# Optimization experiments

Measured on AMD Instinct MI355X. Metric: run time of the kernel, lower is better.

## Reference

```python
import jax, jax.numpy as jnp
import numpy as np

H = 1024     # hidden_size
NH = 16      # num heads
HD = H // NH # head_dim = 64
I = 4096     # intermediate_size
EPS = 1e-6


def rmsnorm(x, w, eps=EPS):
    var = jnp.mean(jnp.square(x), axis=-1, keepdims=True)
    return x * jax.lax.rsqrt(var + eps) * w


def attention(x, ctx, wq, wk, wv, wo):
    # x: [B,S,H], ctx: [B,Skv,H]; weights stored [in,out]
    B, S, _ = x.shape
    Skv = ctx.shape[1]
    q = (x @ wq).reshape(B, S, NH, HD)
    k = (ctx @ wk).reshape(B, Skv, NH, HD)
    v = (ctx @ wv).reshape(B, Skv, NH, HD)
    scores = jnp.einsum('bqhd,bkhd->bhqk', q, k) * (HD ** -0.5)
    attn = jax.nn.softmax(scores.astype(jnp.float32), axis=-1).astype(q.dtype)
    out = jnp.einsum('bhqk,bkhd->bqhd', attn, v).reshape(B, S, NH * HD)
    return out @ wo


def mlp(x, wg, wu, wd):
    return (jax.nn.silu(x @ wg) * (x @ wu)) @ wd


def setup_inputs() -> dict:
    key = jax.random.key(0)
    ks = jax.random.split(key, 16)
    p = lambda k, shape: (jax.random.normal(k, shape, jnp.float32) * 0.02)
    return {
        'hidden_states': jax.random.normal(ks[0], (1, 2048, H), jnp.float32),
        'context': jax.random.normal(ks[1], (1, 2048, H), jnp.float32),
        'sa_norm_w': jnp.ones((H,), jnp.float32),
        'sa_wq': p(ks[2], (H, NH * HD)),
        'sa_wk': p(ks[3], (H, NH * HD)),
        'sa_wv': p(ks[4], (H, NH * HD)),
        'sa_wo': p(ks[5], (NH * HD, H)),
        'ca_norm_w': jnp.ones((H,), jnp.float32),
        'ca_wq': p(ks[6], (H, NH * HD)),
        'ca_wk': p(ks[7], (H, NH * HD)),
        'ca_wv': p(ks[8], (H, NH * HD)),
        'ca_wo': p(ks[9], (NH * HD, H)),
        'mlp_norm_w': jnp.ones((H,), jnp.float32),
        'w_gate': p(ks[10], (H, I)),
        'w_up': p(ks[11], (H, I)),
        'w_down': p(ks[12], (I, H)),
    }


def reference(hidden_states, context, sa_norm_w, sa_wq, sa_wk, sa_wv, sa_wo,
              ca_norm_w, ca_wq, ca_wk, ca_wv, ca_wo,
              mlp_norm_w, w_gate, w_up, w_down):
    # self-attention block
    residual = hidden_states
    h = rmsnorm(hidden_states, sa_norm_w)
    h = residual + attention(h, h, sa_wq, sa_wk, sa_wv, sa_wo)
    # cross-attention block
    residual = h
    hn = rmsnorm(h, ca_norm_w)
    h = residual + attention(hn, context, ca_wq, ca_wk, ca_wv, ca_wo)
    # MLP block
    residual = h
    hn = rmsnorm(h, mlp_norm_w)
    h = residual + mlp(hn, w_gate, w_up, w_down)
    return h
```

## Files before the change

### kernel.cpp

```cpp
#include <hip/hip_runtime.h>

#define H 1024
#define S 2048
#define NH 16
#define HD 64
#define ISZ 4096

typedef __attribute__((ext_vector_type(8))) short s8v;
typedef __attribute__((ext_vector_type(4))) short s4v;
typedef __attribute__((ext_vector_type(4))) float f4v;

__device__ __forceinline__ short f2bf(float f) {
    unsigned u = __builtin_bit_cast(unsigned, f);
    unsigned r = (u + 0x7FFFu + ((u >> 16) & 1u)) >> 16;
    return (short)r;
}
__device__ __forceinline__ float bf2f(short s) {
    unsigned u = ((unsigned)(unsigned short)s) << 16;
    return __builtin_bit_cast(float, u);
}

__device__ __forceinline__ void gload_lds16(const short* g, short* l) {
    __builtin_amdgcn_global_load_lds(
        (const __attribute__((address_space(1))) void*)g,
        (__attribute__((address_space(3))) void*)l, 16, 0, 0);
}

struct PreArgs {
    const void* hid; const void* ctx;
    const void* sanw; const void* canw; const void* mlpnw;
    const void* w[11];
    short* hidc; short* ctxc; short* xn;
    short* canw_o; short* mlpnw_o;
    short* wT[11];
    int* flag_out;
};

__device__ __forceinline__ void tr_tile(const void* src, short* dst, int K, int N,
                                        int k0, int n0, int rmul, int roff,
                                        int isbf, float* tile ) {
    int t = threadIdx.x;
    int c = t & 31, r0 = t >> 5;
    if (isbf) {
        const short* s = (const short*)src;
#pragma unroll
        for (int i = 0; i < 4; i++)
            tile[(r0 + i * 8) * 33 + c] = bf2f(s[(k0 + r0 + i * 8) * N + n0 + c]);
    } else {
        const float* s = (const float*)src;
#pragma unroll
        for (int i = 0; i < 4; i++)
            tile[(r0 + i * 8) * 33 + c] = s[(k0 + r0 + i * 8) * N + n0 + c];
    }
    __syncthreads();
#pragma unroll
    for (int i = 0; i < 4; i++)
        dst[((n0 + r0 + i * 8) * rmul + roff) * K + k0 + c] = f2bf(tile[c * 33 + r0 + i * 8]);
}

__global__ __launch_bounds__(256) void preamble_kernel(PreArgs pa) {
    __shared__ float tile[32 * 33];
    __shared__ float red[4];
    int b = blockIdx.x;
    int t = threadIdx.x;
    int isbf = (((const unsigned*)pa.sanw)[0] == 0x3F803F80u);
    if (blockIdx.x == 0 && t == 0) pa.flag_out[0] = isbf;

    if (b < 2048) {
        int row = b;
        float xf[4];
        if (isbf) {
            s4v xv = *(const s4v*)((const short*)pa.hid + row * H + t * 4);
#pragma unroll
            for (int j = 0; j < 4; j++) xf[j] = bf2f(xv[j]);
        } else {
            const float* s = (const float*)pa.hid + row * H + t * 4;
#pragma unroll
            for (int j = 0; j < 4; j++) xf[j] = s[j];
        }
        float ss = 0.f;
        s4v cv;
#pragma unroll
        for (int j = 0; j < 4; j++) { cv[j] = f2bf(xf[j]); xf[j] = bf2f(cv[j]); ss += xf[j] * xf[j]; }
        *(s4v*)(pa.hidc + row * H + t * 4) = cv;
        int lane = t & 63, wid = t >> 6;
#pragma unroll
        for (int off = 32; off >= 1; off >>= 1) ss += __shfl_xor(ss, off);
        if (lane == 0) red[wid] = ss;
        __syncthreads();
        float tot = red[0] + red[1] + red[2] + red[3];
        float scale = rsqrtf(tot * (1.f / (float)H) + 1e-6f);
        float wv[4];
        if (isbf) {
            s4v wq = *(const s4v*)((const short*)pa.sanw + t * 4);
#pragma unroll
            for (int j = 0; j < 4; j++) wv[j] = bf2f(wq[j]);
        } else {
            const float* s = (const float*)pa.sanw + t * 4;
#pragma unroll
            for (int j = 0; j < 4; j++) wv[j] = s[j];
        }
        s4v ov;
#pragma unroll
        for (int j = 0; j < 4; j++) ov[j] = f2bf(xf[j] * scale * wv[j]);
        *(s4v*)(pa.xn + row * H + t * 4) = ov;
        return;
    }
    b -= 2048;
    if (b < 1024) {
        int i8 = b * 2048 + t * 8;
        if (isbf) {
            *(s8v*)(pa.ctxc + i8) = *(const s8v*)((const short*)pa.ctx + i8);
        } else {
            const float* s = (const float*)pa.ctx;
            s8v o;
#pragma unroll
            for (int j = 0; j < 8; j++) o[j] = f2bf(s[i8 + j]);
            *(s8v*)(pa.ctxc + i8) = o;
        }
        return;
    }
    b -= 1024;
    if (b < 2) {
        const void* src = (b == 0) ? pa.canw : pa.mlpnw;
        short* dst = (b == 0) ? pa.canw_o : pa.mlpnw_o;
        if (isbf) { if (t * 4 < H) *(s4v*)(dst + t * 4) = *(const s4v*)((const short*)src + t * 4); }
        else {
            const float* s = (const float*)src;
            s4v o;
#pragma unroll
            for (int j = 0; j < 4; j++) o[j] = f2bf(s[t * 4 + j]);
            *(s4v*)(dst + t * 4) = o;
        }
        return;
    }
    b -= 2;
    if (b < 8 * 1024) {
        int w = b >> 10, tl = b & 1023;
        tr_tile(pa.w[w], pa.wT[w], H, H, (tl & 31) * 32, (tl >> 5) * 32, 1, 0, isbf, tile);
        return;
    }
    b -= 8 * 1024;
    if (b < 2 * 4096) {
        int w = 8 + (b >> 12), tl = b & 4095;
        tr_tile(pa.w[w], pa.wT[8], H, ISZ, (tl & 31) * 32, (tl >> 5) * 32, 2, w - 8, isbf, tile);
        return;
    }
    b -= 2 * 4096;
    {
        tr_tile(pa.w[10], pa.wT[10], ISZ, H, (b & 127) * 32, (b >> 7) * 32, 1, 0, isbf, tile);
    }
}

__global__ __launch_bounds__(256) void rmsnorm_kernel(const short* __restrict__ x,
                                                      const short* __restrict__ w,
                                                      short* __restrict__ out) {
    int row = blockIdx.x;
    int t = threadIdx.x;
    int lane = t & 63, wid = t >> 6;
    const short* xr = x + row * H;

    s4v xv = *(const s4v*)(xr + t * 4);
    float xf[4];
    float ss = 0.f;
#pragma unroll
    for (int j = 0; j < 4; j++) { xf[j] = bf2f(xv[j]); ss += xf[j] * xf[j]; }
#pragma unroll
    for (int off = 32; off >= 1; off >>= 1) ss += __shfl_xor(ss, off);

    __shared__ float red[4];
    if (lane == 0) red[wid] = ss;
    __syncthreads();
    float tot = red[0] + red[1] + red[2] + red[3];
    float scale = rsqrtf(tot * (1.f / (float)H) + 1e-6f);

    s4v wv = *(const s4v*)(w + t * 4);
    s4v ov;
#pragma unroll
    for (int j = 0; j < 4; j++) ov[j] = f2bf(xf[j] * scale * bf2f(wv[j]));
    *(s4v*)(out + row * H + t * 4) = ov;
}

template <int BM_, int BN_>
__global__ __launch_bounds__(256, 2) void gemm_bt_kernel(
    const short* __restrict__ A0, const short* __restrict__ A1, int split, int lda,
    const short* __restrict__ Bt,
    void* __restrict__ C, int ldc, int K,
    const short* __restrict__ res,
    const int* __restrict__ dtype_flag,
    short* __restrict__ vtbuf, int vcol0,
    short* __restrict__ silu_out) {

    constexpr int MC = BM_ / 32;
    constexpr int NC = BN_ / 32;

    const short* A = (blockIdx.y < split) ? A0 : A1;
    int m0 = blockIdx.x * BM_;
    int n0 = blockIdx.y * BN_;

    __shared__ short As[2 * BM_ * 32];
    __shared__ short Bs[2 * BN_ * 32];

    int t = threadIdx.x;
    int lane = t & 63, wid = t >> 6;
    int quad = lane >> 4, l15 = lane & 15;
    int wr = wid >> 1, wc = wid & 1;

    f4v acc[MC][NC] = {};

    int ld4 = lane >> 2, lc8 = (lane & 3) * 8;

    for (int k0 = 0; k0 < K; k0 += 64) {
#pragma unroll
        for (int h = 0; h < 2; h++) {
#pragma unroll
            for (int i = 0; i < BM_ / 64; i++)
                gload_lds16(A + (m0 + wid * (BM_ / 4) + i * 16 + ld4) * lda + k0 + h * 32 + lc8,
                            As + h * BM_ * 32 + (wid * (BM_ / 4) + i * 16) * 32);
#pragma unroll
            for (int i = 0; i < BN_ / 64; i++)
                gload_lds16(Bt + (n0 + wid * (BN_ / 4) + i * 16 + ld4) * K + k0 + h * 32 + lc8,
                            Bs + h * BN_ * 32 + (wid * (BN_ / 4) + i * 16) * 32);
        }
        __syncthreads();

#pragma unroll
        for (int h = 0; h < 2; h++) {
            s8v af[MC], bfv[NC];
#pragma unroll
            for (int mc = 0; mc < MC; mc++)
                af[mc] = *(const s8v*)(As + h * BM_ * 32 + (wr * (BM_ / 2) + mc * 16 + l15) * 32 + quad * 8);
#pragma unroll
            for (int nc = 0; nc < NC; nc++)
                bfv[nc] = *(const s8v*)(Bs + h * BN_ * 32 + (wc * (BN_ / 2) + nc * 16 + l15) * 32 + quad * 8);

#pragma unroll
            for (int mc = 0; mc < MC; mc++)
#pragma unroll
                for (int nc = 0; nc < NC; nc++)
                    acc[mc][nc] = __builtin_amdgcn_mfma_f32_16x16x32_bf16(af[mc], bfv[nc], acc[mc][nc], 0, 0, 0);
        }
        __syncthreads();
    }

    if (silu_out) {
#pragma unroll
        for (int mc = 0; mc < MC; mc++) {
#pragma unroll
            for (int nc = 0; nc < NC; nc++) {
                int row = m0 + wr * (BM_ / 2) + mc * 16 + quad * 4;
                int col = n0 + wc * (BN_ / 2) + nc * 16 + l15;
#pragma unroll
                for (int r = 0; r < 4; r++) {
                    float v = acc[mc][nc][r];
                    float other = __shfl_xor(v, 1);
                    if ((l15 & 1) == 0) {
                        float sig = 1.f / (1.f + __expf(-v));
                        silu_out[(row + r) * ISZ + (col >> 1)] = f2bf(v * sig * other);
                    }
                }
            }
        }
        return;
    }

    int out_fp32 = (dtype_flag != nullptr) && (dtype_flag[0] == 0);

#pragma unroll
    for (int mc = 0; mc < MC; mc++) {
#pragma unroll
        for (int nc = 0; nc < NC; nc++) {
            int row = m0 + wr * (BM_ / 2) + mc * 16 + quad * 4;
            int col = n0 + wc * (BN_ / 2) + nc * 16 + l15;
#pragma unroll
            for (int r = 0; r < 4; r++) {
                float vf = acc[mc][nc][r];
                if (res) vf += bf2f(res[(row + r) * ldc + col]);
                if (vtbuf && col >= vcol0)
                    vtbuf[(col - vcol0) * S + row + r] = f2bf(vf);
                else if (out_fp32)
                    ((float*)C)[(row + r) * ldc + col] = vf;
                else
                    ((short*)C)[(row + r) * ldc + col] = f2bf(vf);
            }
        }
    }
}

__global__ __launch_bounds__(256) void flash_attn_kernel(const short* __restrict__ q,
                                                         const short* __restrict__ k,
                                                         const short* __restrict__ vt,
                                                         int rs,
                                                         short* __restrict__ o) {
    int h = blockIdx.y;
    int q0 = blockIdx.x * 64;
    int t = threadIdx.x;
    int lane = t & 63, wid = t >> 6;
    int quad = lane >> 4, l15 = lane & 15;

    __shared__ short K2[2 * 128 * 32];
    __shared__ short V2[4 * 64 * 32];
    __shared__ short Pw[4][2048];

    int ld4 = lane >> 2, lc8 = (lane & 3) * 8;

    s8v bq[2];
    int qrow = q0 + wid * 16 + l15;
#pragma unroll
    for (int c = 0; c < 2; c++) {
        s8v raw = *(const s8v*)(q + qrow * rs + h * HD + c * 32 + quad * 8);
#pragma unroll
        for (int j = 0; j < 8; j++) bq[c][j] = f2bf(0.125f * bf2f(raw[j]));
    }

    f4v o_acc[4] = {};
    float m_s = -INFINITY, l_s = 0.f;

    for (int kv0 = 0; kv0 < S; kv0 += 128) {
#pragma unroll
        for (int dc = 0; dc < 2; dc++)
#pragma unroll
            for (int i = 0; i < 2; i++)
                gload_lds16(k + (kv0 + wid * 32 + i * 16 + ld4) * rs + h * HD + dc * 32 + lc8,
                            K2 + dc * 4096 + (wid * 32 + i * 16) * 32);
#pragma unroll
        for (int kc2 = 0; kc2 < 4; kc2++)
            gload_lds16(vt + (h * HD + wid * 16 + ld4) * S + kv0 + kc2 * 32 + lc8,
                        V2 + kc2 * 2048 + (wid * 16) * 32);
        __syncthreads();

        f4v st[8];
#pragma unroll
        for (int kc = 0; kc < 8; kc++) {
            f4v a_ = (f4v){0.f, 0.f, 0.f, 0.f};
#pragma unroll
            for (int dc = 0; dc < 2; dc++) {
                s8v kf = *(const s8v*)(K2 + dc * 4096 + (kc * 16 + l15) * 32 + quad * 8);
                a_ = __builtin_amdgcn_mfma_f32_16x16x32_bf16(kf, bq[dc], a_, 0, 0, 0);
            }
            st[kc] = a_;
        }

        float mloc = -INFINITY;
#pragma unroll
        for (int kc = 0; kc < 8; kc++)
#pragma unroll
            for (int r = 0; r < 4; r++) mloc = fmaxf(mloc, st[kc][r]);
        mloc = fmaxf(mloc, __shfl_xor(mloc, 16));
        mloc = fmaxf(mloc, __shfl_xor(mloc, 32));
        float m_new = fmaxf(m_s, mloc);
        float alpha = __expf(m_s - m_new);
        float lloc = 0.f;
#pragma unroll
        for (int kc = 0; kc < 8; kc++)
#pragma unroll
            for (int r = 0; r < 4; r++) {
                float p = __expf(st[kc][r] - m_new);
                st[kc][r] = p;
                lloc += p;
            }
        lloc += __shfl_xor(lloc, 16);
        lloc += __shfl_xor(lloc, 32);
        l_s = l_s * alpha + lloc;
        m_s = m_new;
#pragma unroll
        for (int nd = 0; nd < 4; nd++)
#pragma unroll
            for (int r = 0; r < 4; r++) o_acc[nd][r] *= alpha;

#pragma unroll
        for (int kc = 0; kc < 8; kc++)
#pragma unroll
            for (int r = 0; r < 4; r++)
                Pw[wid][(kc >> 1) * 512 + l15 * 32 + (kc & 1) * 16 + quad * 4 + r] = f2bf(st[kc][r]);

#pragma unroll
        for (int nd = 0; nd < 4; nd++) {
#pragma unroll
            for (int kc2 = 0; kc2 < 4; kc2++) {
                s8v vf = *(const s8v*)(V2 + kc2 * 2048 + (nd * 16 + l15) * 32 + quad * 8);
                s8v pf = *(const s8v*)(Pw[wid] + kc2 * 512 + l15 * 32 + quad * 8);
                o_acc[nd] = __builtin_amdgcn_mfma_f32_16x16x32_bf16(vf, pf, o_acc[nd], 0, 0, 0);
            }
        }
        __syncthreads();
    }

    float inv = 1.f / l_s;
#pragma unroll
    for (int nd = 0; nd < 4; nd++)
#pragma unroll
        for (int r = 0; r < 4; r++)
            Pw[wid][l15 * 64 + nd * 16 + quad * 4 + r] = f2bf(o_acc[nd][r] * inv);

    int qr = lane >> 2, dc2 = (lane & 3) * 16;
    s8v x0 = *(const s8v*)(Pw[wid] + qr * 64 + dc2);
    s8v x1 = *(const s8v*)(Pw[wid] + qr * 64 + dc2 + 8);
    short* dst = o + (q0 + wid * 16 + qr) * H + h * HD + dc2;
    *(s8v*)(dst) = x0;
    *(s8v*)(dst + 8) = x1;
}

extern "C" void kernel_launch(void* const* d_in, const int* in_sizes, int n_in,
                              void* d_out, int out_size, void* d_ws, size_t ws_size,
                              hipStream_t stream) {
    const int SH = S * H;
    const int WH = H * H;
    const int WI = H * ISZ;

    int* flag = (int*)d_ws;
    short* base = (short*)d_ws + 16;

    short* hidc   = base;
    short* ctxc   = hidc + SH;
    short* sanw   = ctxc + SH;
    short* canw   = sanw + H;
    short* mlpnw  = canw + H;
    short* saqkvT = mlpnw + H;
    short* sawoT  = saqkvT + 3 * WH;
    short* caqkvT = sawoT + WH;
    short* cawoT  = caqkvT + 3 * WH;
    short* wguT   = cawoT + WH;
    short* wdT    = wguT + 2 * WI;
    short* xn     = wdT + WI;
    short* qkv    = xn + SH;
    short* ao     = qkv + 3 * SH;
    short* h1     = ao + SH;
    short* gu     = qkv;
    short* h2     = qkv + 8 * SH;
    short* vt     = h2 + SH;

    dim3 blk(256);

    PreArgs pa;
    pa.hid = d_in[0]; pa.ctx = d_in[1];
    pa.sanw = d_in[2]; pa.canw = d_in[7]; pa.mlpnw = d_in[12];
    const void* wsrc[11] = {d_in[3], d_in[4], d_in[5], d_in[6],
                            d_in[8], d_in[9], d_in[10], d_in[11],
                            d_in[13], d_in[14], d_in[15]};
    short* wdst[11] = {saqkvT, saqkvT + WH, saqkvT + 2 * WH, sawoT,
                       caqkvT, caqkvT + WH, caqkvT + 2 * WH, cawoT,
                       wguT, wguT , wdT};
    for (int i = 0; i < 11; i++) { pa.w[i] = wsrc[i]; pa.wT[i] = wdst[i]; }
    pa.hidc = hidc; pa.ctxc = ctxc; pa.xn = xn;
    pa.canw_o = canw; pa.mlpnw_o = mlpnw;
    pa.flag_out = flag;
    const int pre_blocks = 2048 + 1024 + 2 + 8 * 1024 + 2 * 4096 + 4096;
    preamble_kernel<<<pre_blocks, blk, 0, stream>>>(pa);

    gemm_bt_kernel<64, 128><<<dim3(S / 64, 3 * H / 128), blk, 0, stream>>>(
        xn, xn, 24, H, saqkvT, qkv, 3 * H, H, nullptr, nullptr, vt, 2 * H, nullptr);
    flash_attn_kernel<<<dim3(S / 64, NH), blk, 0, stream>>>(qkv, qkv + H, vt, 3 * H, ao);
    gemm_bt_kernel<64, 64><<<dim3(S / 64, H / 64), blk, 0, stream>>>(
        ao, ao, 16, H, sawoT, h1, H, H, hidc, nullptr, nullptr, 0, nullptr);

    rmsnorm_kernel<<<S, blk, 0, stream>>>(h1, canw, xn);
    gemm_bt_kernel<64, 128><<<dim3(S / 64, 3 * H / 128), blk, 0, stream>>>(
        xn, ctxc, 8, H, caqkvT, qkv, 3 * H, H, nullptr, nullptr, vt, 2 * H, nullptr);
    flash_attn_kernel<<<dim3(S / 64, NH), blk, 0, stream>>>(qkv, qkv + H, vt, 3 * H, ao);
    gemm_bt_kernel<64, 64><<<dim3(S / 64, H / 64), blk, 0, stream>>>(
        ao, ao, 16, H, cawoT, h2, H, H, h1, nullptr, nullptr, 0, nullptr);

    rmsnorm_kernel<<<S, blk, 0, stream>>>(h2, mlpnw, xn);
    gemm_bt_kernel<128, 128><<<dim3(S / 128, 2 * ISZ / 128), blk, 0, stream>>>(
        xn, xn, 64, H, wguT, nullptr, 2 * ISZ, H, nullptr, nullptr, nullptr, 0, gu);
    gemm_bt_kernel<64, 64><<<dim3(S / 64, H / 64), blk, 0, stream>>>(
        gu, gu, 16, ISZ, wdT, d_out, H, ISZ, h2, flag, nullptr, 0, nullptr);
}
```

Before: 499.3 us.

## Double-buffer GEMM LDS tiles, use 8-wave blocks and larger tiles

Rewrites the GEMM kernel to use 512-thread blocks with a 2x4 wave layout and a double-buffered LDS ping-pong. The next K-tile is loaded while the current one is computed, so there is one barrier per iteration instead of two. Tile sizes grow at every call site (128x128 for QKV, 64x128 for the out/down projections, 256x256 for gate/up). The goal is to hide global-load latency and raise data reuse per block. The cost is more LDS and register pressure per block: 256x256 needs 128 KB of LDS plus 32 accumulator tiles per wave, which may cut occupancy or exceed the LDS limit. The larger tiles also give fewer blocks for the small GEMMs.

```diff
diff --git a/kernel.cpp b/kernel.cpp
--- a/kernel.cpp
+++ b/kernel.cpp
@@ -182,7 +182,7 @@
 }
 
 template <int BM_, int BN_>
-__global__ __launch_bounds__(256, 2) void gemm_bt_kernel(
+__global__ __launch_bounds__(512, 2) void gemm_bt_kernel(
     const short* __restrict__ A0, const short* __restrict__ A1, int split, int lda,
     const short* __restrict__ Bt,
     void* __restrict__ C, int ldc, int K,
@@ -192,56 +192,73 @@
     short* __restrict__ silu_out) {
 
     constexpr int MC = BM_ / 32;
-    constexpr int NC = BN_ / 32;
+    constexpr int NC = BN_ / 64;
+    constexpr int U  = (BM_ + BN_) / 8;
+    constexpr int PT = U / 8;
+    constexpr int BUF = (BM_ + BN_) * 64;
+
+    __shared__ short lds[2 * BUF];
 
     const short* A = (blockIdx.y < split) ? A0 : A1;
     int m0 = blockIdx.x * BM_;
     int n0 = blockIdx.y * BN_;
 
-    __shared__ short As[2 * BM_ * 32];
-    __shared__ short Bs[2 * BN_ * 32];
-
     int t = threadIdx.x;
     int lane = t & 63, wid = t >> 6;
     int quad = lane >> 4, l15 = lane & 15;
-    int wr = wid >> 1, wc = wid & 1;
+    int wr = wid >> 2, wc = wid & 3;
+    int ld4 = lane >> 2, lc8 = (lane & 3) * 8;
 
     f4v acc[MC][NC] = {};
 
-    int ld4 = lane >> 2, lc8 = (lane & 3) * 8;
-
-    for (int k0 = 0; k0 < K; k0 += 64) {
-#pragma unroll
-        for (int h = 0; h < 2; h++) {
-#pragma unroll
-            for (int i = 0; i < BM_ / 64; i++)
-                gload_lds16(A + (m0 + wid * (BM_ / 4) + i * 16 + ld4) * lda + k0 + h * 32 + lc8,
-                            As + h * BM_ * 32 + (wid * (BM_ / 4) + i * 16) * 32);
-#pragma unroll
-            for (int i = 0; i < BN_ / 64; i++)
-                gload_lds16(Bt + (n0 + wid * (BN_ / 4) + i * 16 + ld4) * K + k0 + h * 32 + lc8,
-                            Bs + h * BN_ * 32 + (wid * (BN_ / 4) + i * 16) * 32);
-        }
+    auto stage = [&](short* buf, int k0) {
+#pragma unroll
+        for (int s = 0; s < PT; ++s) {
+            int u = wid * PT + s;
+            if (u < BM_ / 8) {
+                int h = u / (BM_ / 16), r16 = u % (BM_ / 16);
+                gload_lds16(A + (m0 + r16 * 16 + ld4) * lda + k0 + h * 32 + lc8,
+                            buf + h * (BM_ * 32) + r16 * 512);
+            } else {
+                int ub = u - BM_ / 8;
+                int h = ub / (BN_ / 16), r16 = ub % (BN_ / 16);
+                gload_lds16(Bt + (n0 + r16 * 16 + ld4) * K + k0 + h * 32 + lc8,
+                            buf + BM_ * 64 + h * (BN_ * 32) + r16 * 512);
+            }
+        }
+    };
+
+    auto compute = [&](const short* buf) {
+#pragma unroll
+        for (int kh = 0; kh < 2; ++kh) {
+            s8v af[MC], bfv[NC];
+#pragma unroll
+            for (int mc = 0; mc < MC; ++mc)
+                af[mc] = *(const s8v*)(buf + kh * (BM_ * 32) +
+                                       (wr * (BM_ / 2) + mc * 16 + l15) * 32 + quad * 8);
+#pragma unroll
+            for (int nc = 0; nc < NC; ++nc)
+                bfv[nc] = *(const s8v*)(buf + BM_ * 64 + kh * (BN_ * 32) +
+                                        (wc * (BN_ / 4) + nc * 16 + l15) * 32 + quad * 8);
+#pragma unroll
+            for (int mc = 0; mc < MC; ++mc)
+#pragma unroll
+                for (int nc = 0; nc < NC; ++nc)
+                    acc[mc][nc] = __builtin_amdgcn_mfma_f32_16x16x32_bf16(af[mc], bfv[nc], acc[mc][nc], 0, 0, 0);
+        }
+    };
+
+    const int KT = K / 64;
+    stage(lds, 0);
+    __syncthreads();
+    int cur = 0;
+    for (int kt = 0; kt < KT - 1; ++kt) {
+        stage(lds + (cur ^ 1) * BUF, (kt + 1) * 64);
+        compute(lds + cur * BUF);
         __syncthreads();
-
-#pragma unroll
-        for (int h = 0; h < 2; h++) {
-            s8v af[MC], bfv[NC];
-#pragma unroll
-            for (int mc = 0; mc < MC; mc++)
-                af[mc] = *(const s8v*)(As + h * BM_ * 32 + (wr * (BM_ / 2) + mc * 16 + l15) * 32 + quad * 8);
-#pragma unroll
-            for (int nc = 0; nc < NC; nc++)
-                bfv[nc] = *(const s8v*)(Bs + h * BN_ * 32 + (wc * (BN_ / 2) + nc * 16 + l15) * 32 + quad * 8);
-
-#pragma unroll
-            for (int mc = 0; mc < MC; mc++)
-#pragma unroll
-                for (int nc = 0; nc < NC; nc++)
-                    acc[mc][nc] = __builtin_amdgcn_mfma_f32_16x16x32_bf16(af[mc], bfv[nc], acc[mc][nc], 0, 0, 0);
-        }
-        __syncthreads();
-    }
+        cur ^= 1;
+    }
+    compute(lds + cur * BUF);
 
     if (silu_out) {
 #pragma unroll
@@ -249,7 +266,7 @@
 #pragma unroll
             for (int nc = 0; nc < NC; nc++) {
                 int row = m0 + wr * (BM_ / 2) + mc * 16 + quad * 4;
-                int col = n0 + wc * (BN_ / 2) + nc * 16 + l15;
+                int col = n0 + wc * (BN_ / 4) + nc * 16 + l15;
 #pragma unroll
                 for (int r = 0; r < 4; r++) {
                     float v = acc[mc][nc][r];
@@ -271,7 +288,7 @@
 #pragma unroll
         for (int nc = 0; nc < NC; nc++) {
             int row = m0 + wr * (BM_ / 2) + mc * 16 + quad * 4;
-            int col = n0 + wc * (BN_ / 2) + nc * 16 + l15;
+            int col = n0 + wc * (BN_ / 4) + nc * 16 + l15;
 #pragma unroll
             for (int r = 0; r < 4; r++) {
                 float vf = acc[mc][nc][r];
@@ -431,6 +448,7 @@
     short* vt     = h2 + SH;
 
     dim3 blk(256);
+    dim3 blk2(512);
 
     PreArgs pa;
     pa.hid = d_in[0]; pa.ctx = d_in[1];
@@ -448,22 +466,22 @@
     const int pre_blocks = 2048 + 1024 + 2 + 8 * 1024 + 2 * 4096 + 4096;
     preamble_kernel<<<pre_blocks, blk, 0, stream>>>(pa);
 
-    gemm_bt_kernel<64, 128><<<dim3(S / 64, 3 * H / 128), blk, 0, stream>>>(
+    gemm_bt_kernel<128, 128><<<dim3(S / 128, 3 * H / 128), blk2, 0, stream>>>(
         xn, xn, 24, H, saqkvT, qkv, 3 * H, H, nullptr, nullptr, vt, 2 * H, nullptr);
     flash_attn_kernel<<<dim3(S / 64, NH), blk, 0, stream>>>(qkv, qkv + H, vt, 3 * H, ao);
-    gemm_bt_kernel<64, 64><<<dim3(S / 64, H / 64), blk, 0, stream>>>(
-        ao, ao, 16, H, sawoT, h1, H, H, hidc, nullptr, nullptr, 0, nullptr);
+    gemm_bt_kernel<64, 128><<<dim3(S / 64, H / 128), blk2, 0, stream>>>(
+        ao, ao, 8, H, sawoT, h1, H, H, hidc, nullptr, nullptr, 0, nullptr);
 
     rmsnorm_kernel<<<S, blk, 0, stream>>>(h1, canw, xn);
-    gemm_bt_kernel<64, 128><<<dim3(S / 64, 3 * H / 128), blk, 0, stream>>>(
+    gemm_bt_kernel<128, 128><<<dim3(S / 128, 3 * H / 128), blk2, 0, stream>>>(
         xn, ctxc, 8, H, caqkvT, qkv, 3 * H, H, nullptr, nullptr, vt, 2 * H, nullptr);
     flash_attn_kernel<<<dim3(S / 64, NH), blk, 0, stream>>>(qkv, qkv + H, vt, 3 * H, ao);
-    gemm_bt_kernel<64, 64><<<dim3(S / 64, H / 64), blk, 0, stream>>>(
-        ao, ao, 16, H, cawoT, h2, H, H, h1, nullptr, nullptr, 0, nullptr);
+    gemm_bt_kernel<64, 128><<<dim3(S / 64, H / 128), blk2, 0, stream>>>(
+        ao, ao, 8, H, cawoT, h2, H, H, h1, nullptr, nullptr, 0, nullptr);
 
     rmsnorm_kernel<<<S, blk, 0, stream>>>(h2, mlpnw, xn);
-    gemm_bt_kernel<128, 128><<<dim3(S / 128, 2 * ISZ / 128), blk, 0, stream>>>(
-        xn, xn, 64, H, wguT, nullptr, 2 * ISZ, H, nullptr, nullptr, nullptr, 0, gu);
-    gemm_bt_kernel<64, 64><<<dim3(S / 64, H / 64), blk, 0, stream>>>(
-        gu, gu, 16, ISZ, wdT, d_out, H, ISZ, h2, flag, nullptr, 0, nullptr);
-}
+    gemm_bt_kernel<256, 256><<<dim3(S / 256, 2 * ISZ / 256), blk2, 0, stream>>>(
+        xn, xn, 32, H, wguT, nullptr, 2 * ISZ, H, nullptr, nullptr, nullptr, 0, gu);
+    gemm_bt_kernel<64, 128><<<dim3(S / 64, H / 128), blk2, 0, stream>>>(
+        gu, gu, 8, ISZ, wdT, d_out, H, ISZ, h2, flag, nullptr, 0, nullptr);
+}
```

Result: faster. 484.7 us (-2.9%).
